# Optimization experiments

Measured on AMD Instinct MI355X. Metric: run time of the kernel, lower is better.

## Reference

```python
import jax, jax.numpy as jnp
import numpy as np

N_NODES = 50000
N_EDGES = 1600000
NODE_DIM = 1024
HID = 128
OUT = 128
LN_EPS = 1e-5


def setup_inputs() -> dict:
    key = jax.random.key(0)
    ks = jax.random.split(key, 8)
    s = lambda d: 1.0 / np.sqrt(d)
    return {
        "x": jax.random.normal(ks[0], (N_NODES, NODE_DIM), jnp.float32),
        "edge_index": jax.random.randint(ks[1], (2, N_EDGES), 0, N_NODES, jnp.int64),
        "proj_w": jax.random.normal(ks[2], (HID, NODE_DIM), jnp.float32) * s(NODE_DIM),
        "proj_b": jnp.zeros((HID,), jnp.float32),
        "lin_l_w": jax.random.normal(ks[3], (HID, HID), jnp.float32) * s(HID),
        "lin_l_b": jnp.zeros((HID,), jnp.float32),
        "lin_r_w": jax.random.normal(ks[4], (HID, HID), jnp.float32) * s(HID),
        "ln_g": jnp.ones((HID,), jnp.float32),
        "ln_b": jnp.zeros((HID,), jnp.float32),
        "out_w": jax.random.normal(ks[5], (OUT, HID), jnp.float32) * s(HID),
        "out_b": jnp.zeros((OUT,), jnp.float32),
    }


def reference(x, edge_index, proj_w, proj_b, lin_l_w, lin_l_b, lin_r_w, ln_g, ln_b, out_w, out_b):
    n = x.shape[0]
    # input projection + ReLU: [N, node_dim] -> [N, H]
    h = jax.nn.relu(x @ proj_w.T + proj_b)
    # SAGEConv(mean): gather source features, mean-scatter to targets
    src, dst = edge_index[0], edge_index[1]
    agg = jax.ops.segment_sum(h[src], dst, num_segments=n)  # [N, H]
    deg = jax.ops.segment_sum(jnp.ones((src.shape[0],), h.dtype), dst, num_segments=n)
    mean_nbr = agg / jnp.maximum(deg, 1.0)[:, None]
    h = mean_nbr @ lin_l_w.T + lin_l_b + h @ lin_r_w.T
    # LayerNorm over feature dim
    mu = h.mean(-1, keepdims=True)
    var = jnp.mean((h - mu) ** 2, -1, keepdims=True)
    h = (h - mu) * jax.lax.rsqrt(var + LN_EPS) * ln_g + ln_b
    h = jax.nn.relu(h)  # dropout is identity in eval
    # batch=None -> global mean pool over all nodes: [1, H]
    g = h.mean(0, keepdims=True)
    return g @ out_w.T + out_b
```

## Files before the change

kernel.cpp:

```cpp
#include <hip/hip_runtime.h>

#define N_NODES  50000
#define N_EDGES  1600000
#define NODE_DIM 1024
#define HID      128
#define LN_EPS   1e-5f
#define NBUCK    196
#define SHARD    6250

typedef float f32x4 __attribute__((ext_vector_type(4)));
typedef __bf16 bf16x8 __attribute__((ext_vector_type(8)));
typedef unsigned short u16x8 __attribute__((ext_vector_type(8)));
typedef unsigned int u32x4 __attribute__((ext_vector_type(4)));

__device__ __forceinline__ unsigned short f2bf(float f) {
  __bf16 b = (__bf16)f;
  return __builtin_bit_cast(unsigned short, b);
}
__device__ __forceinline__ unsigned int pkbf(float a, float b) {
  return (unsigned int)f2bf(a) | ((unsigned int)f2bf(b) << 16);
}
__device__ __forceinline__ float bf2f(unsigned short v) {
  return __uint_as_float((unsigned int)v << 16);
}

__device__ __forceinline__ int scan256_excl(int v, int buf[2][256], int t) {
  int cur = 0;
  buf[0][t] = v;
  __syncthreads();
  for (int off = 1; off < 256; off <<= 1) {
    int nxt = cur ^ 1;
    int s = buf[cur][t];
    if (t >= off) s += buf[cur][t - off];
    buf[nxt][t] = s;
    cur = nxt;
    __syncthreads();
  }
  return buf[cur][t] - v;
}

__global__ __launch_bounds__(256) void k_wpack(const float* __restrict__ w,
                                               unsigned short* __restrict__ wp) {
  int idx = blockIdx.x * 256 + threadIdx.x;
  int lane = idx & 63;
  int n = (idx >> 6) & 7;
  int ks = idx >> 9;
  int fr = lane & 15, kg = lane >> 4;
  const float* src = w + (size_t)(n * 16 + fr) * NODE_DIM + ks * 32 + kg * 8;
  float4 v0 = *(const float4*)(src);
  float4 v1 = *(const float4*)(src + 4);
  unsigned int* o = (unsigned int*)(wp + (size_t)idx * 8);
  o[0] = pkbf(v0.x, v0.y);
  o[1] = pkbf(v0.z, v0.w);
  o[2] = pkbf(v1.x, v1.y);
  o[3] = pkbf(v1.z, v1.w);
}

__global__ __launch_bounds__(256, 3) void k_proj(const float* __restrict__ x,
                                                 const unsigned short* __restrict__ wp,
                                                 const float* __restrict__ pb,
                                                 unsigned short* __restrict__ h) {
  const int wave = threadIdx.x >> 6, lane = threadIdx.x & 63;
  const int fr = lane & 15, kg = lane >> 4;
  const int strip = blockIdx.x * 4 + wave;
  const int m0 = strip * 32;

  int r0 = m0 + fr;      if (r0 >= N_NODES) r0 = N_NODES - 1;
  int r1 = m0 + 16 + fr; if (r1 >= N_NODES) r1 = N_NODES - 1;
  const float* a0p = x + (size_t)r0 * NODE_DIM + kg * 8;
  const float* a1p = x + (size_t)r1 * NODE_DIM + kg * 8;
  const bf16x8* bp = (const bf16x8*)wp + lane;

  f32x4 acc[2][8] = {};

  float4 xa0, xa1, xa2, xa3;
  float4 ya0, ya1, ya2, ya3;

#define LOADA_X(KS) { const float* p0 = a0p + (KS) * 32; const float* p1 = a1p + (KS) * 32; \
  xa0 = *(const float4*)p0; xa1 = *(const float4*)(p0 + 4); \
  xa2 = *(const float4*)p1; xa3 = *(const float4*)(p1 + 4); }
#define LOADA_Y(KS) { const float* p0 = a0p + (KS) * 32; const float* p1 = a1p + (KS) * 32; \
  ya0 = *(const float4*)p0; ya1 = *(const float4*)(p0 + 4); \
  ya2 = *(const float4*)p1; ya3 = *(const float4*)(p1 + 4); }

#define COMPUTE(A0, A1, A2, A3, KS) { \
  bf16x8 bfv[8]; \
  _Pragma("unroll") \
  for (int n = 0; n < 8; n++) bfv[n] = bp[((KS) * 8 + n) * 64]; \
  u32x4 pa0, pa1; \
  pa0[0] = pkbf(A0.x, A0.y); pa0[1] = pkbf(A0.z, A0.w); \
  pa0[2] = pkbf(A1.x, A1.y); pa0[3] = pkbf(A1.z, A1.w); \
  pa1[0] = pkbf(A2.x, A2.y); pa1[1] = pkbf(A2.z, A2.w); \
  pa1[2] = pkbf(A3.x, A3.y); pa1[3] = pkbf(A3.z, A3.w); \
  bf16x8 af0 = __builtin_bit_cast(bf16x8, pa0); \
  bf16x8 af1 = __builtin_bit_cast(bf16x8, pa1); \
  _Pragma("unroll") \
  for (int n = 0; n < 8; n++) { \
    acc[0][n] = __builtin_amdgcn_mfma_f32_16x16x32_bf16(af0, bfv[n], acc[0][n], 0, 0, 0); \
    acc[1][n] = __builtin_amdgcn_mfma_f32_16x16x32_bf16(af1, bfv[n], acc[1][n], 0, 0, 0); \
  } }

  LOADA_X(0);
  for (int ks = 0; ks < 32; ks += 2) {
    LOADA_Y(ks + 1);
    COMPUTE(xa0, xa1, xa2, xa3, ks);
    if (ks + 2 < 32) LOADA_X(ks + 2);
    COMPUTE(ya0, ya1, ya2, ya3, ks + 1);
  }
#undef LOADA_X
#undef LOADA_Y
#undef COMPUTE

  const int cr = (lane >> 4) * 4, cc = lane & 15;
#pragma unroll
  for (int n = 0; n < 8; n++) {
    const int col = n * 16 + cc;
    const float bias = pb[col];
#pragma unroll
    for (int m = 0; m < 2; m++) {
      const int rowb = m0 + m * 16 + cr;
#pragma unroll
      for (int i = 0; i < 4; i++) {
        float v = acc[m][n][i] + bias;
        h[(size_t)(rowb + i) * HID + col] = f2bf(v > 0.f ? v : 0.f);
      }
    }
  }
}

__global__ __launch_bounds__(256) void k_hist(const int* __restrict__ ei,
                                              int* __restrict__ counts) {
  __shared__ int bins[NBUCK];
  int t = threadIdx.x;
  if (t < NBUCK) bins[t] = 0;
  __syncthreads();
  int base = blockIdx.x * SHARD;
  for (int i = t; i < SHARD; i += 256)
    atomicAdd(&bins[ei[N_EDGES + base + i] >> 8], 1);
  __syncthreads();
  if (t < NBUCK) counts[t * 256 + blockIdx.x] = bins[t];
}

__global__ __launch_bounds__(256) void k_s1(const int* __restrict__ counts,
                                            int* __restrict__ basem,
                                            int* __restrict__ btot) {
  __shared__ int buf[2][256];
  int t = threadIdx.x, b = blockIdx.x;
  int v = counts[b * 256 + t];
  int excl = scan256_excl(v, buf, t);
  basem[b * 256 + t] = excl;
  if (t == 255) btot[b] = excl + v;
}

__global__ __launch_bounds__(256) void k_s2(const int* __restrict__ btot,
                                            int* __restrict__ bstart,
                                            float* __restrict__ accum) {
  __shared__ int buf[2][256];
  int t = threadIdx.x;
  int v = (t < NBUCK) ? btot[t] : 0;
  int excl = scan256_excl(v, buf, t);
  if (t < NBUCK) bstart[t] = excl;
  if (t == 0) bstart[NBUCK] = N_EDGES;
  if (t < HID) accum[t] = 0.f;
}

__global__ __launch_bounds__(256) void k_scatter(const int* __restrict__ ei,
                                                 const int* __restrict__ basem,
                                                 const int* __restrict__ bstart,
                                                 unsigned int* __restrict__ bs) {
  __shared__ int cur[NBUCK];
  int t = threadIdx.x;
  if (t < NBUCK) cur[t] = bstart[t] + basem[t * 256 + blockIdx.x];
  __syncthreads();
  int base = blockIdx.x * SHARD;
  for (int i = t; i < SHARD; i += 256) {
    int e = base + i;
    unsigned int src = (unsigned int)ei[e];
    unsigned int dst = (unsigned int)ei[N_EDGES + e];
    int pos = atomicAdd(&cur[dst >> 8], 1);
    bs[pos] = src | ((dst & 255u) << 16);
  }
}

__global__ __launch_bounds__(256) void k_bucket(const int* __restrict__ bstart,
                                                const unsigned int* __restrict__ bs,
                                                unsigned short* __restrict__ nbr,
                                                int* __restrict__ offs,
                                                int* __restrict__ deg) {
  __shared__ int bins[256];
  __shared__ int buf[2][256];
  __shared__ int curs[256];
  int t = threadIdx.x, b = blockIdx.x;
  int s = bstart[b], e = bstart[b + 1];
  bins[t] = 0;
  __syncthreads();
  for (int i = s + t; i < e; i += 256)
    atomicAdd(&bins[(bs[i] >> 16) & 255u], 1);
  __syncthreads();
  int v = bins[t];
  int excl = scan256_excl(v, buf, t);
  int node = b * 256 + t;
  deg[node]  = v;
  offs[node] = s + excl;
  curs[t]    = s + excl;
  __syncthreads();
  for (int i = s + t; i < e; i += 256) {
    unsigned int p = bs[i];
    int pos = atomicAdd(&curs[(p >> 16) & 255u], 1);
    nbr[pos] = (unsigned short)(p & 0xffffu);
  }
}

__global__ __launch_bounds__(256) void k_gather(const unsigned short* __restrict__ h,
                                                const unsigned short* __restrict__ nbr,
                                                const int* __restrict__ offs,
                                                const int* __restrict__ deg,
                                                unsigned short* __restrict__ mn) {
  const int wave = threadIdx.x >> 6;
  const int lane = threadIdx.x & 63;
  const int node = blockIdx.x * 4 + wave;
  if (node >= N_NODES) return;
  const int g = lane >> 4, li = lane & 15;
  const int d  = deg[node];
  const int st = offs[node];
  float a[8] = {0.f, 0.f, 0.f, 0.f, 0.f, 0.f, 0.f, 0.f};
  int n = g;
  for (; n + 4 < d; n += 8) {
    int s0 = nbr[st + n];
    int s1 = nbr[st + n + 4];
    u16x8 v0 = *(const u16x8*)(h + (size_t)s0 * HID + li * 8);
    u16x8 v1 = *(const u16x8*)(h + (size_t)s1 * HID + li * 8);
#pragma unroll
    for (int k = 0; k < 8; k++) a[k] += bf2f(v0[k]) + bf2f(v1[k]);
  }
  if (n < d) {
    int s0 = nbr[st + n];
    u16x8 v0 = *(const u16x8*)(h + (size_t)s0 * HID + li * 8);
#pragma unroll
    for (int k = 0; k < 8; k++) a[k] += bf2f(v0[k]);
  }
#pragma unroll
  for (int k = 0; k < 8; k++) {
    a[k] += __shfl_xor(a[k], 16);
    a[k] += __shfl_xor(a[k], 32);
  }
  if (g == 0) {
    float inv = 1.f / fmaxf((float)d, 1.f);
    u16x8 r;
#pragma unroll
    for (int k = 0; k < 8; k++) r[k] = f2bf(a[k] * inv);
    *(u16x8*)(mn + (size_t)node * HID + li * 8) = r;
  }
}

__global__ __launch_bounds__(256) void k_sage(const unsigned short* __restrict__ mn,
                                              const unsigned short* __restrict__ h,
                                              const float* __restrict__ wl,
                                              const float* __restrict__ wr,
                                              const float* __restrict__ lb,
                                              const float* __restrict__ lg,
                                              const float* __restrict__ lbt,
                                              float* __restrict__ accum) {
  __shared__ unsigned short As[128 * 32];
  __shared__ unsigned short Bs[128 * 32];
  __shared__ float T3[32 * 128];
  __shared__ float red[4][128];
  const int tid = threadIdx.x;
  const int m0 = blockIdx.x * 128;
  const int wave = tid >> 6, lane = tid & 63;
  const int wm = (wave >> 1) * 64, wn = (wave & 1) * 64;
  const int srow = tid >> 1, scol = (tid & 1) * 16;
  const int fr = lane & 15, ko = (lane >> 4) * 8;

  f32x4 acc[4][4] = {};

  for (int k0 = 0; k0 < 2 * HID; k0 += 32) {
    const unsigned short* baseA = (k0 < HID) ? mn : h;
    const float* baseB = (k0 < HID) ? wl : wr;
    const int kk = (k0 & (HID - 1)) + scol;
    const int arow = m0 + srow;
    u16x8 a0 = {0, 0, 0, 0, 0, 0, 0, 0}, a1 = a0;
    if (arow < N_NODES) {
      const u16x8* p = (const u16x8*)(baseA + (size_t)arow * HID + kk);
      a0 = p[0]; a1 = p[1];
    }
    const float4* q = (const float4*)(baseB + (size_t)srow * HID + kk);
    float4 b0 = q[0], b1 = q[1], b2 = q[2], b3 = q[3];

    __syncthreads();
    *(u16x8*)&As[srow * 32 + scol]     = a0;
    *(u16x8*)&As[srow * 32 + scol + 8] = a1;
    unsigned int* db = (unsigned int*)&Bs[srow * 32 + scol];
    db[0] = pkbf(b0.x, b0.y); db[1] = pkbf(b0.z, b0.w);
    db[2] = pkbf(b1.x, b1.y); db[3] = pkbf(b1.z, b1.w);
    db[4] = pkbf(b2.x, b2.y); db[5] = pkbf(b2.z, b2.w);
    db[6] = pkbf(b3.x, b3.y); db[7] = pkbf(b3.z, b3.w);
    __syncthreads();

    bf16x8 af[4], bfr[4];
#pragma unroll
    for (int m = 0; m < 4; m++)
      af[m] = *(const bf16x8*)&As[(wm + m * 16 + fr) * 32 + ko];
#pragma unroll
    for (int n = 0; n < 4; n++)
      bfr[n] = *(const bf16x8*)&Bs[(wn + n * 16 + fr) * 32 + ko];
#pragma unroll
    for (int m = 0; m < 4; m++)
#pragma unroll
      for (int n = 0; n < 4; n++)
        acc[m][n] = __builtin_amdgcn_mfma_f32_16x16x32_bf16(af[m], bfr[n], acc[m][n], 0, 0, 0);
  }

  const int cr = (lane >> 4) * 4, cc = lane & 15;
  const int p = wave >> 1;
  const float g0 = lg[lane], g1 = lg[lane + 64];
  const float t0 = lbt[lane], t1 = lbt[lane + 64];
  float ax = 0.f, ay = 0.f;
#pragma unroll
  for (int m = 0; m < 4; m++) {
    __syncthreads();
#pragma unroll
    for (int n = 0; n < 4; n++) {
      const int col = wn + n * 16 + cc;
      const float bias = lb[col];
#pragma unroll
      for (int i = 0; i < 4; i++)
        T3[(p * 16 + cr + i) * 128 + col] = acc[m][n][i] + bias;
    }
    __syncthreads();
    for (int r8 = 0; r8 < 8; r8++) {
      int q8 = wave * 8 + r8;
      int grow = m0 + (q8 >> 4) * 64 + m * 16 + (q8 & 15);
      float v0 = T3[q8 * 128 + lane];
      float v1 = T3[q8 * 128 + lane + 64];
      float sum = v0 + v1, ss = v0 * v0 + v1 * v1;
#pragma unroll
      for (int off = 32; off > 0; off >>= 1) {
        sum += __shfl_xor(sum, off);
        ss  += __shfl_xor(ss, off);
      }
      float mu  = sum * (1.f / HID);
      float var = ss * (1.f / HID) - mu * mu;
      float rinv = rsqrtf(var + LN_EPS);
      if (grow < N_NODES) {
        float y0 = (v0 - mu) * rinv * g0 + t0;
        float y1 = (v1 - mu) * rinv * g1 + t1;
        ax += fmaxf(y0, 0.f);
        ay += fmaxf(y1, 0.f);
      }
    }
  }
  red[wave][lane]      = ax;
  red[wave][lane + 64] = ay;
  __syncthreads();
  if (wave == 0) {
    float a  = red[0][lane] + red[1][lane] + red[2][lane] + red[3][lane];
    float bb = red[0][lane + 64] + red[1][lane + 64] + red[2][lane + 64] + red[3][lane + 64];
    atomicAdd(&accum[lane], a);
    atomicAdd(&accum[lane + 64], bb);
  }
}

__global__ __launch_bounds__(128) void k_final(const float* __restrict__ accum,
                                               const float* __restrict__ ow,
                                               const float* __restrict__ ob,
                                               float* __restrict__ out) {
  __shared__ float gs[HID];
  int t = threadIdx.x;
  gs[t] = accum[t] * (1.f / N_NODES);
  __syncthreads();
  float s = ob[t];
  for (int k = 0; k < HID; k++) s += gs[k] * ow[t * HID + k];
  out[t] = s;
}

extern "C" void kernel_launch(void* const* d_in, const int* in_sizes, int n_in,
                              void* d_out, int out_size, void* d_ws, size_t ws_size,
                              hipStream_t stream) {
  const float* x   = (const float*)d_in[0];
  const int*   ei  = (const int*)d_in[1];
  const float* pw  = (const float*)d_in[2];
  const float* pb  = (const float*)d_in[3];
  const float* wl  = (const float*)d_in[4];
  const float* lb  = (const float*)d_in[5];
  const float* wr  = (const float*)d_in[6];
  const float* lg  = (const float*)d_in[7];
  const float* lbt = (const float*)d_in[8];
  const float* ow  = (const float*)d_in[9];
  const float* ob  = (const float*)d_in[10];
  float* out = (float*)d_out;

  const int PAD = NBUCK * 256;
  unsigned short* h  = (unsigned short*)d_ws;
  unsigned short* mn = h + (size_t)PAD * HID;
  unsigned int* bsp  = (unsigned int*)(mn + (size_t)PAD * HID);
  unsigned short* nbr = (unsigned short*)(bsp + N_EDGES);
  int* counts = (int*)(nbr + N_EDGES);
  int* basem  = counts + NBUCK * 256;
  int* btot   = basem + NBUCK * 256;
  int* bstart = btot + 256;
  int* offs   = bstart + 256;
  int* deg    = offs + PAD;
  float* accum = (float*)(deg + PAD);
  unsigned short* wp = (unsigned short*)(accum + 128);

  const int MB  = (N_NODES + 127) / 128;
  const int PB  = (N_NODES + 127) / 128;
  (void)PB;

  hipLaunchKernelGGL(k_wpack,   dim3(64),    dim3(256), 0, stream, pw, wp);
  hipLaunchKernelGGL(k_hist,    dim3(256),   dim3(256), 0, stream, ei, counts);
  hipLaunchKernelGGL(k_s1,      dim3(NBUCK), dim3(256), 0, stream, counts, basem, btot);
  hipLaunchKernelGGL(k_s2,      dim3(1),     dim3(256), 0, stream, btot, bstart, accum);
  hipLaunchKernelGGL(k_scatter, dim3(256),   dim3(256), 0, stream, ei, basem, bstart, bsp);
  hipLaunchKernelGGL(k_bucket,  dim3(NBUCK), dim3(256), 0, stream, bstart, bsp, nbr, offs, deg);
  hipLaunchKernelGGL(k_proj,    dim3(392),   dim3(256), 0, stream, x, wp, pb, h);
  hipLaunchKernelGGL(k_gather,  dim3((N_NODES + 3) / 4), dim3(256), 0, stream, h, nbr, offs, deg, mn);
  hipLaunchKernelGGL(k_sage,    dim3(MB),    dim3(256), 0, stream, mn, h, wl, wr, lb, lg, lbt, accum);
  hipLaunchKernelGGL(k_final,   dim3(1),     dim3(128), 0, stream, accum, ow, ob, out);
}
```

Measured before the change: 473.6 us.

## Replace bucketed CSR build with global-atomic CSR and register-only SAGE GEMM

Result: slower. 619.2 us (+30.7%).

```diff
diff --git a/kernel.cpp b/kernel.cpp
--- a/kernel.cpp
+++ b/kernel.cpp
@@ -6,7 +6,8 @@
 #define HID      128
 #define LN_EPS   1e-5f
 #define NBUCK    196
-#define SHARD    6250
+#define PAD      (NBUCK * 256)
+#define PSTRIPS  1568
 
 typedef float f32x4 __attribute__((ext_vector_type(4)));
 typedef __bf16 bf16x8 __attribute__((ext_vector_type(8)));
@@ -37,6 +38,33 @@
     __syncthreads();
   }
   return buf[cur][t] - v;
+}
+
+__global__ __launch_bounds__(256) void k_wspack(const float* __restrict__ wl,
+                                                const float* __restrict__ wr,
+                                                unsigned short* __restrict__ wsp,
+                                                int* __restrict__ deg,
+                                                float* __restrict__ accum) {
+  int idx = blockIdx.x * 256 + threadIdx.x;
+  int4* d4 = (int4*)deg;
+  for (int j = idx; j < PAD / 4; j += 4096) d4[j] = make_int4(0, 0, 0, 0);
+  if (idx < HID) accum[idx] = 0.f;
+
+  int lane = idx & 63;
+  int n = (idx >> 6) & 7;
+  int ks = idx >> 9;
+  int fr = lane & 15, kg = lane >> 4;
+  int row = n * 16 + fr;
+  int k0 = ks * 32 + kg * 8;
+  const float* src = (k0 < HID) ? (wl + (size_t)row * HID + k0)
+                                : (wr + (size_t)row * HID + (k0 - HID));
+  float4 v0 = *(const float4*)(src);
+  float4 v1 = *(const float4*)(src + 4);
+  unsigned int* o = (unsigned int*)(wsp + (size_t)idx * 8);
+  o[0] = pkbf(v0.x, v0.y);
+  o[1] = pkbf(v0.z, v0.w);
+  o[2] = pkbf(v1.x, v1.y);
+  o[3] = pkbf(v1.z, v1.w);
 }
 
 __global__ __launch_bounds__(256) void k_wpack(const float* __restrict__ w,
@@ -56,25 +84,68 @@
   o[3] = pkbf(v1.z, v1.w);
 }
 
-__global__ __launch_bounds__(256, 3) void k_proj(const float* __restrict__ x,
-                                                 const unsigned short* __restrict__ wp,
-                                                 const float* __restrict__ pb,
-                                                 unsigned short* __restrict__ h) {
-  const int wave = threadIdx.x >> 6, lane = threadIdx.x & 63;
+__global__ __launch_bounds__(256) void k_deg(const int* __restrict__ ei,
+                                             int* __restrict__ deg) {
+  int t = blockIdx.x * 256 + threadIdx.x;
+  for (int e = t; e < N_EDGES; e += gridDim.x * 256)
+    atomicAdd(&deg[ei[N_EDGES + e]], 1);
+}
+
+__global__ __launch_bounds__(256) void k_scan1(const int* __restrict__ deg,
+                                               int* __restrict__ offs,
+                                               int* __restrict__ btot) {
+  __shared__ int buf[2][256];
+  int t = threadIdx.x, b = blockIdx.x;
+  int v = deg[b * 256 + t];
+  int excl = scan256_excl(v, buf, t);
+  offs[b * 256 + t] = excl;
+  if (t == 255) btot[b] = excl + v;
+}
+
+__global__ __launch_bounds__(256) void k_scan2(const int* __restrict__ btot,
+                                               int* __restrict__ bstart) {
+  __shared__ int buf[2][256];
+  int t = threadIdx.x;
+  int v = (t < NBUCK) ? btot[t] : 0;
+  int excl = scan256_excl(v, buf, t);
+  if (t < NBUCK) bstart[t] = excl;
+}
+
+__global__ __launch_bounds__(256) void k_curinit(const int* __restrict__ bstart,
+                                                 int* __restrict__ offs,
+                                                 int* __restrict__ cur) {
+  int node = blockIdx.x * 256 + threadIdx.x;
+  int o = offs[node] + bstart[node >> 8];
+  offs[node] = o;
+  cur[node] = o;
+}
+
+__global__ __launch_bounds__(256) void k_fill(const int* __restrict__ ei,
+                                              int* __restrict__ cur,
+                                              unsigned short* __restrict__ nbr) {
+  int t = blockIdx.x * 256 + threadIdx.x;
+  for (int e = t; e < N_EDGES; e += gridDim.x * 256) {
+    int src = ei[e];
+    int dst = ei[N_EDGES + e];
+    int pos = atomicAdd(&cur[dst], 1);
+    nbr[pos] = (unsigned short)src;
+  }
+}
+
+__device__ __forceinline__ void proj_strip(const float* __restrict__ x,
+                                           const unsigned short* __restrict__ wp,
+                                           const float* __restrict__ pb,
+                                           unsigned short* __restrict__ h,
+                                           int strip, int lane) {
   const int fr = lane & 15, kg = lane >> 4;
-  const int strip = blockIdx.x * 4 + wave;
-  const int m0 = strip * 32;
-
-  int r0 = m0 + fr;      if (r0 >= N_NODES) r0 = N_NODES - 1;
-  int r1 = m0 + 16 + fr; if (r1 >= N_NODES) r1 = N_NODES - 1;
+  const int m0s = strip * 32;
+  int r0 = m0s + fr;      if (r0 >= N_NODES) r0 = N_NODES - 1;
+  int r1 = m0s + 16 + fr; if (r1 >= N_NODES) r1 = N_NODES - 1;
   const float* a0p = x + (size_t)r0 * NODE_DIM + kg * 8;
   const float* a1p = x + (size_t)r1 * NODE_DIM + kg * 8;
   const bf16x8* bp = (const bf16x8*)wp + lane;
-
   f32x4 acc[2][8] = {};
-
-  float4 xa0, xa1, xa2, xa3;
-  float4 ya0, ya1, ya2, ya3;
+  float4 xa0, xa1, xa2, xa3, ya0, ya1, ya2, ya3;
 
 #define LOADA_X(KS) { const float* p0 = a0p + (KS) * 32; const float* p1 = a1p + (KS) * 32; \
   xa0 = *(const float4*)p0; xa1 = *(const float4*)(p0 + 4); \
@@ -82,7 +153,6 @@
 #define LOADA_Y(KS) { const float* p0 = a0p + (KS) * 32; const float* p1 = a1p + (KS) * 32; \
   ya0 = *(const float4*)p0; ya1 = *(const float4*)(p0 + 4); \
   ya2 = *(const float4*)p1; ya3 = *(const float4*)(p1 + 4); }
-
 #define COMPUTE(A0, A1, A2, A3, KS) { \
   bf16x8 bfv[8]; \
   _Pragma("unroll") \
@@ -118,7 +188,7 @@
     const float bias = pb[col];
 #pragma unroll
     for (int m = 0; m < 2; m++) {
-      const int rowb = m0 + m * 16 + cr;
+      const int rowb = m0s + m * 16 + cr;
 #pragma unroll
       for (int i = 0; i < 4; i++) {
         float v = acc[m][n][i] + bias;
@@ -128,87 +198,11 @@
   }
 }
 
-__global__ __launch_bounds__(256) void k_hist(const int* __restrict__ ei,
-                                              int* __restrict__ counts) {
-  __shared__ int bins[NBUCK];
-  int t = threadIdx.x;
-  if (t < NBUCK) bins[t] = 0;
-  __syncthreads();
-  int base = blockIdx.x * SHARD;
-  for (int i = t; i < SHARD; i += 256)
-    atomicAdd(&bins[ei[N_EDGES + base + i] >> 8], 1);
-  __syncthreads();
-  if (t < NBUCK) counts[t * 256 + blockIdx.x] = bins[t];
-}
-
-__global__ __launch_bounds__(256) void k_s1(const int* __restrict__ counts,
-                                            int* __restrict__ basem,
-                                            int* __restrict__ btot) {
-  __shared__ int buf[2][256];
-  int t = threadIdx.x, b = blockIdx.x;
-  int v = counts[b * 256 + t];
-  int excl = scan256_excl(v, buf, t);
-  basem[b * 256 + t] = excl;
-  if (t == 255) btot[b] = excl + v;
-}
-
-__global__ __launch_bounds__(256) void k_s2(const int* __restrict__ btot,
-                                            int* __restrict__ bstart,
-                                            float* __restrict__ accum) {
-  __shared__ int buf[2][256];
-  int t = threadIdx.x;
-  int v = (t < NBUCK) ? btot[t] : 0;
-  int excl = scan256_excl(v, buf, t);
-  if (t < NBUCK) bstart[t] = excl;
-  if (t == 0) bstart[NBUCK] = N_EDGES;
-  if (t < HID) accum[t] = 0.f;
-}
-
-__global__ __launch_bounds__(256) void k_scatter(const int* __restrict__ ei,
-                                                 const int* __restrict__ basem,
-                                                 const int* __restrict__ bstart,
-                                                 unsigned int* __restrict__ bs) {
-  __shared__ int cur[NBUCK];
-  int t = threadIdx.x;
-  if (t < NBUCK) cur[t] = bstart[t] + basem[t * 256 + blockIdx.x];
-  __syncthreads();
-  int base = blockIdx.x * SHARD;
-  for (int i = t; i < SHARD; i += 256) {
-    int e = base + i;
-    unsigned int src = (unsigned int)ei[e];
-    unsigned int dst = (unsigned int)ei[N_EDGES + e];
-    int pos = atomicAdd(&cur[dst >> 8], 1);
-    bs[pos] = src | ((dst & 255u) << 16);
-  }
-}
-
-__global__ __launch_bounds__(256) void k_bucket(const int* __restrict__ bstart,
-                                                const unsigned int* __restrict__ bs,
-                                                unsigned short* __restrict__ nbr,
-                                                int* __restrict__ offs,
-                                                int* __restrict__ deg) {
-  __shared__ int bins[256];
-  __shared__ int buf[2][256];
-  __shared__ int curs[256];
-  int t = threadIdx.x, b = blockIdx.x;
-  int s = bstart[b], e = bstart[b + 1];
-  bins[t] = 0;
-  __syncthreads();
-  for (int i = s + t; i < e; i += 256)
-    atomicAdd(&bins[(bs[i] >> 16) & 255u], 1);
-  __syncthreads();
-  int v = bins[t];
-  int excl = scan256_excl(v, buf, t);
-  int node = b * 256 + t;
-  deg[node]  = v;
-  offs[node] = s + excl;
-  curs[t]    = s + excl;
-  __syncthreads();
-  for (int i = s + t; i < e; i += 256) {
-    unsigned int p = bs[i];
-    int pos = atomicAdd(&curs[(p >> 16) & 255u], 1);
-    nbr[pos] = (unsigned short)(p & 0xffffu);
-  }
+__global__ __launch_bounds__(256, 3) void k_proj(const float* __restrict__ x,
+                                                 const unsigned short* __restrict__ wp,
+                                                 const float* __restrict__ pb,
+                                                 unsigned short* __restrict__ h) {
+  proj_strip(x, wp, pb, h, blockIdx.x * 4 + (threadIdx.x >> 6), threadIdx.x & 63);
 }
 
 __global__ __launch_bounds__(256) void k_gather(const unsigned short* __restrict__ h,
@@ -219,21 +213,25 @@
   const int wave = threadIdx.x >> 6;
   const int lane = threadIdx.x & 63;
   const int node = blockIdx.x * 4 + wave;
-  if (node >= N_NODES) return;
   const int g = lane >> 4, li = lane & 15;
   const int d  = deg[node];
   const int st = offs[node];
   float a[8] = {0.f, 0.f, 0.f, 0.f, 0.f, 0.f, 0.f, 0.f};
   int n = g;
-  for (; n + 4 < d; n += 8) {
+  for (; n + 12 < d; n += 16) {
     int s0 = nbr[st + n];
     int s1 = nbr[st + n + 4];
+    int s2 = nbr[st + n + 8];
+    int s3 = nbr[st + n + 12];
     u16x8 v0 = *(const u16x8*)(h + (size_t)s0 * HID + li * 8);
     u16x8 v1 = *(const u16x8*)(h + (size_t)s1 * HID + li * 8);
-#pragma unroll
-    for (int k = 0; k < 8; k++) a[k] += bf2f(v0[k]) + bf2f(v1[k]);
-  }
-  if (n < d) {
+    u16x8 v2 = *(const u16x8*)(h + (size_t)s2 * HID + li * 8);
+    u16x8 v3 = *(const u16x8*)(h + (size_t)s3 * HID + li * 8);
+#pragma unroll
+    for (int k = 0; k < 8; k++)
+      a[k] += (bf2f(v0[k]) + bf2f(v1[k])) + (bf2f(v2[k]) + bf2f(v3[k]));
+  }
+  for (; n < d; n += 4) {
     int s0 = nbr[st + n];
     u16x8 v0 = *(const u16x8*)(h + (size_t)s0 * HID + li * 8);
 #pragma unroll
@@ -255,109 +253,94 @@
 
 __global__ __launch_bounds__(256) void k_sage(const unsigned short* __restrict__ mn,
                                               const unsigned short* __restrict__ h,
-                                              const float* __restrict__ wl,
-                                              const float* __restrict__ wr,
+                                              const unsigned short* __restrict__ wsp,
                                               const float* __restrict__ lb,
                                               const float* __restrict__ lg,
                                               const float* __restrict__ lbt,
                                               float* __restrict__ accum) {
-  __shared__ unsigned short As[128 * 32];
-  __shared__ unsigned short Bs[128 * 32];
-  __shared__ float T3[32 * 128];
   __shared__ float red[4][128];
-  const int tid = threadIdx.x;
-  const int m0 = blockIdx.x * 128;
-  const int wave = tid >> 6, lane = tid & 63;
-  const int wm = (wave >> 1) * 64, wn = (wave & 1) * 64;
-  const int srow = tid >> 1, scol = (tid & 1) * 16;
-  const int fr = lane & 15, ko = (lane >> 4) * 8;
-
-  f32x4 acc[4][4] = {};
-
-  for (int k0 = 0; k0 < 2 * HID; k0 += 32) {
-    const unsigned short* baseA = (k0 < HID) ? mn : h;
-    const float* baseB = (k0 < HID) ? wl : wr;
-    const int kk = (k0 & (HID - 1)) + scol;
-    const int arow = m0 + srow;
-    u16x8 a0 = {0, 0, 0, 0, 0, 0, 0, 0}, a1 = a0;
-    if (arow < N_NODES) {
-      const u16x8* p = (const u16x8*)(baseA + (size_t)arow * HID + kk);
-      a0 = p[0]; a1 = p[1];
+  const int wave = threadIdx.x >> 6, lane = threadIdx.x & 63;
+  const int strip = blockIdx.x * 4 + wave;
+  const int m0s = strip * 32;
+  const int fr = lane & 15, kg = lane >> 4;
+  const bf16x8* bp = (const bf16x8*)wsp + lane;
+
+  const unsigned short* a0m = mn + (size_t)(m0s + fr) * HID + kg * 8;
+  const unsigned short* a1m = mn + (size_t)(m0s + 16 + fr) * HID + kg * 8;
+  const unsigned short* a0h = h  + (size_t)(m0s + fr) * HID + kg * 8;
+  const unsigned short* a1h = h  + (size_t)(m0s + 16 + fr) * HID + kg * 8;
+
+  f32x4 acc[2][8] = {};
+#pragma unroll
+  for (int ks = 0; ks < 8; ks++) {
+    const unsigned short* s0 = (ks < 4) ? (a0m + ks * 32) : (a0h + (ks - 4) * 32);
+    const unsigned short* s1 = (ks < 4) ? (a1m + ks * 32) : (a1h + (ks - 4) * 32);
+    bf16x8 af0 = *(const bf16x8*)s0;
+    bf16x8 af1 = *(const bf16x8*)s1;
+    bf16x8 bfv[8];
+#pragma unroll
+    for (int n = 0; n < 8; n++) bfv[n] = bp[(ks * 8 + n) * 64];
+#pragma unroll
+    for (int n = 0; n < 8; n++) {
+      acc[0][n] = __builtin_amdgcn_mfma_f32_16x16x32_bf16(af0, bfv[n], acc[0][n], 0, 0, 0);
+      acc[1][n] = __builtin_amdgcn_mfma_f32_16x16x32_bf16(af1, bfv[n], acc[1][n], 0, 0, 0);
     }
-    const float4* q = (const float4*)(baseB + (size_t)srow * HID + kk);
-    float4 b0 = q[0], b1 = q[1], b2 = q[2], b3 = q[3];
-
-    __syncthreads();
-    *(u16x8*)&As[srow * 32 + scol]     = a0;
-    *(u16x8*)&As[srow * 32 + scol + 8] = a1;
-    unsigned int* db = (unsigned int*)&Bs[srow * 32 + scol];
-    db[0] = pkbf(b0.x, b0.y); db[1] = pkbf(b0.z, b0.w);
-    db[2] = pkbf(b1.x, b1.y); db[3] = pkbf(b1.z, b1.w);
-    db[4] = pkbf(b2.x, b2.y); db[5] = pkbf(b2.z, b2.w);
-    db[6] = pkbf(b3.x, b3.y); db[7] = pkbf(b3.z, b3.w);
-    __syncthreads();
-
-    bf16x8 af[4], bfr[4];
-#pragma unroll
-    for (int m = 0; m < 4; m++)
-      af[m] = *(const bf16x8*)&As[(wm + m * 16 + fr) * 32 + ko];
-#pragma unroll
-    for (int n = 0; n < 4; n++)
-      bfr[n] = *(const bf16x8*)&Bs[(wn + n * 16 + fr) * 32 + ko];
-#pragma unroll
-    for (int m = 0; m < 4; m++)
-#pragma unroll
-      for (int n = 0; n < 4; n++)
-        acc[m][n] = __builtin_amdgcn_mfma_f32_16x16x32_bf16(af[m], bfr[n], acc[m][n], 0, 0, 0);
   }
 
   const int cr = (lane >> 4) * 4, cc = lane & 15;
-  const int p = wave >> 1;
-  const float g0 = lg[lane], g1 = lg[lane + 64];
-  const float t0 = lbt[lane], t1 = lbt[lane + 64];
-  float ax = 0.f, ay = 0.f;
-#pragma unroll
-  for (int m = 0; m < 4; m++) {
-    __syncthreads();
-#pragma unroll
-    for (int n = 0; n < 4; n++) {
-      const int col = wn + n * 16 + cc;
-      const float bias = lb[col];
-#pragma unroll
-      for (int i = 0; i < 4; i++)
-        T3[(p * 16 + cr + i) * 128 + col] = acc[m][n][i] + bias;
-    }
-    __syncthreads();
-    for (int r8 = 0; r8 < 8; r8++) {
-      int q8 = wave * 8 + r8;
-      int grow = m0 + (q8 >> 4) * 64 + m * 16 + (q8 & 15);
-      float v0 = T3[q8 * 128 + lane];
-      float v1 = T3[q8 * 128 + lane + 64];
-      float sum = v0 + v1, ss = v0 * v0 + v1 * v1;
-#pragma unroll
-      for (int off = 32; off > 0; off >>= 1) {
+  float gv[8], bv[8], lbv[8];
+#pragma unroll
+  for (int n = 0; n < 8; n++) {
+    gv[n]  = lg[n * 16 + cc];
+    bv[n]  = lbt[n * 16 + cc];
+    lbv[n] = lb[n * 16 + cc];
+  }
+  float pool[8] = {0.f, 0.f, 0.f, 0.f, 0.f, 0.f, 0.f, 0.f};
+#pragma unroll
+  for (int m = 0; m < 2; m++) {
+#pragma unroll
+    for (int i = 0; i < 4; i++) {
+      float v[8];
+      float sum = 0.f, ss = 0.f;
+#pragma unroll
+      for (int n = 0; n < 8; n++) {
+        v[n] = acc[m][n][i] + lbv[n];
+        sum += v[n];
+        ss  += v[n] * v[n];
+      }
+#pragma unroll
+      for (int off = 1; off < 16; off <<= 1) {
         sum += __shfl_xor(sum, off);
         ss  += __shfl_xor(ss, off);
       }
-      float mu  = sum * (1.f / HID);
-      float var = ss * (1.f / HID) - mu * mu;
+      float mu   = sum * (1.f / HID);
+      float var  = ss * (1.f / HID) - mu * mu;
       float rinv = rsqrtf(var + LN_EPS);
-      if (grow < N_NODES) {
-        float y0 = (v0 - mu) * rinv * g0 + t0;
-        float y1 = (v1 - mu) * rinv * g1 + t1;
-        ax += fmaxf(y0, 0.f);
-        ay += fmaxf(y1, 0.f);
+      int row = m0s + m * 16 + cr + i;
+      if (row < N_NODES) {
+#pragma unroll
+        for (int n = 0; n < 8; n++) {
+          float y = (v[n] - mu) * rinv * gv[n] + bv[n];
+          pool[n] += fmaxf(y, 0.f);
+        }
       }
     }
   }
-  red[wave][lane]      = ax;
-  red[wave][lane + 64] = ay;
+#pragma unroll
+  for (int n = 0; n < 8; n++) {
+    pool[n] += __shfl_xor(pool[n], 16);
+    pool[n] += __shfl_xor(pool[n], 32);
+  }
+  if (lane < 16) {
+#pragma unroll
+    for (int n = 0; n < 8; n++) red[wave][n * 16 + lane] = pool[n];
+  }
   __syncthreads();
   if (wave == 0) {
-    float a  = red[0][lane] + red[1][lane] + red[2][lane] + red[3][lane];
-    float bb = red[0][lane + 64] + red[1][lane + 64] + red[2][lane + 64] + red[3][lane + 64];
-    atomicAdd(&accum[lane], a);
-    atomicAdd(&accum[lane + 64], bb);
+    float s0 = red[0][lane] + red[1][lane] + red[2][lane] + red[3][lane];
+    float s1 = red[0][lane + 64] + red[1][lane + 64] + red[2][lane + 64] + red[3][lane + 64];
+    atomicAdd(&accum[lane], s0);
+    atomicAdd(&accum[lane + 64], s1);
   }
 }
 
@@ -390,32 +373,27 @@
   const float* ob  = (const float*)d_in[10];
   float* out = (float*)d_out;
 
-  const int PAD = NBUCK * 256;
   unsigned short* h  = (unsigned short*)d_ws;
   unsigned short* mn = h + (size_t)PAD * HID;
-  unsigned int* bsp  = (unsigned int*)(mn + (size_t)PAD * HID);
-  unsigned short* nbr = (unsigned short*)(bsp + N_EDGES);
-  int* counts = (int*)(nbr + N_EDGES);
-  int* basem  = counts + NBUCK * 256;
-  int* btot   = basem + NBUCK * 256;
+  unsigned short* nbr = mn + (size_t)PAD * HID;
+  int* deg    = (int*)(nbr + N_EDGES);
+  int* offs   = deg + PAD;
+  int* cur    = offs + PAD;
+  int* btot   = cur + PAD;
   int* bstart = btot + 256;
-  int* offs   = bstart + 256;
-  int* deg    = offs + PAD;
-  float* accum = (float*)(deg + PAD);
-  unsigned short* wp = (unsigned short*)(accum + 128);
-
-  const int MB  = (N_NODES + 127) / 128;
-  const int PB  = (N_NODES + 127) / 128;
-  (void)PB;
-
-  hipLaunchKernelGGL(k_wpack,   dim3(64),    dim3(256), 0, stream, pw, wp);
-  hipLaunchKernelGGL(k_hist,    dim3(256),   dim3(256), 0, stream, ei, counts);
-  hipLaunchKernelGGL(k_s1,      dim3(NBUCK), dim3(256), 0, stream, counts, basem, btot);
-  hipLaunchKernelGGL(k_s2,      dim3(1),     dim3(256), 0, stream, btot, bstart, accum);
-  hipLaunchKernelGGL(k_scatter, dim3(256),   dim3(256), 0, stream, ei, basem, bstart, bsp);
-  hipLaunchKernelGGL(k_bucket,  dim3(NBUCK), dim3(256), 0, stream, bstart, bsp, nbr, offs, deg);
-  hipLaunchKernelGGL(k_proj,    dim3(392),   dim3(256), 0, stream, x, wp, pb, h);
-  hipLaunchKernelGGL(k_gather,  dim3((N_NODES + 3) / 4), dim3(256), 0, stream, h, nbr, offs, deg, mn);
-  hipLaunchKernelGGL(k_sage,    dim3(MB),    dim3(256), 0, stream, mn, h, wl, wr, lb, lg, lbt, accum);
-  hipLaunchKernelGGL(k_final,   dim3(1),     dim3(128), 0, stream, accum, ow, ob, out);
-}
+  float* accum = (float*)(bstart + 256);
+  unsigned short* wp  = (unsigned short*)(accum + 128);
+  unsigned short* wsp = wp + (size_t)HID * NODE_DIM;
+
+  hipLaunchKernelGGL(k_wspack,  dim3(16),        dim3(256), 0, stream, wl, wr, wsp, deg, accum);
+  hipLaunchKernelGGL(k_wpack,   dim3(64),        dim3(256), 0, stream, pw, wp);
+  hipLaunchKernelGGL(k_deg,     dim3(800),       dim3(256), 0, stream, ei, deg);
+  hipLaunchKernelGGL(k_scan1,   dim3(NBUCK),     dim3(256), 0, stream, deg, offs, btot);
+  hipLaunchKernelGGL(k_scan2,   dim3(1),         dim3(256), 0, stream, btot, bstart);
+  hipLaunchKernelGGL(k_curinit, dim3(NBUCK),     dim3(256), 0, stream, bstart, offs, cur);
+  hipLaunchKernelGGL(k_fill,    dim3(800),       dim3(256), 0, stream, ei, cur, nbr);
+  hipLaunchKernelGGL(k_proj,    dim3(PSTRIPS/4), dim3(256), 0, stream, x, wp, pb, h);
+  hipLaunchKernelGGL(k_gather,  dim3(PAD/4),     dim3(256), 0, stream, h, nbr, offs, deg, mn);
+  hipLaunchKernelGGL(k_sage,    dim3(PSTRIPS/4), dim3(256), 0, stream, mn, h, wsp, lb, lg, lbt, accum);
+  hipLaunchKernelGGL(k_final,   dim3(1),         dim3(128), 0, stream, accum, ow, ob, out);
+}
```
